# Performance work log

Hardware: AMD Instinct MI355X
Metric: run time of the kernel (lower is better)

The kernel has to match this reference:

```python
import jax, jax.numpy as jnp
import numpy as np

K = 3  # kernel size for all locally-connected layers

def lc2d(x, w, b, stride):
    """Locally connected 2d: per-output-location unshared weights.
    x: [B, C, H, W]; w: [1, O, C, Ho, Wo, K*K]; b: [1, O, Ho, Wo].
    Matches torch: x.unfold(2,K,s).unfold(3,K,s) -> [B,C,Ho,Wo,K,K] flattened
    to K*K, then (x[:,None]*w).sum([2,-1]) + b.
    """
    # patches: [B, C*K*K, Ho, Wo], feature order (c, kh, kw) == torch unfold order
    p = jax.lax.conv_general_dilated_patches(x, (K, K), (stride, stride), 'VALID')
    B, CKK, Ho, Wo = p.shape
    C = w.shape[2]
    p = p.reshape(B, C, K * K, Ho, Wo)
    out = jnp.einsum('bckhw,ochwk->bohw', p, w[0])
    return out + b

def setup_inputs() -> dict:
    key = jax.random.key(0)
    ks = jax.random.split(key, 11)
    s = 0.1
    return {
        'x':   jax.random.normal(ks[0], (8192, 1, 28, 28), dtype=jnp.float32),
        'w1':  jax.random.normal(ks[1], (1, 16, 1, 13, 13, 9), dtype=jnp.float32) * s,
        'b1':  jax.random.normal(ks[2], (1, 16, 13, 13), dtype=jnp.float32) * s,
        'w2':  jax.random.normal(ks[3], (1, 32, 16, 6, 6, 9), dtype=jnp.float32) * s,
        'b2':  jax.random.normal(ks[4], (1, 32, 6, 6), dtype=jnp.float32) * s,
        'w3':  jax.random.normal(ks[5], (1, 64, 32, 4, 4, 9), dtype=jnp.float32) * s,
        'b3':  jax.random.normal(ks[6], (1, 64, 4, 4), dtype=jnp.float32) * s,
        'fw1': jax.random.normal(ks[7], (512, 1024), dtype=jnp.float32) * 0.03,
        'fb1': jax.random.normal(ks[8], (512,), dtype=jnp.float32) * 0.03,
        'fw2': jax.random.normal(ks[9], (10, 512), dtype=jnp.float32) * 0.03,
        'fb2': jax.random.normal(ks[10], (10,), dtype=jnp.float32) * 0.03,
    }

def reference(x, w1, b1, w2, b2, w3, b3, fw1, fb1, fw2, fb2):
    h = jax.nn.relu(lc2d(x, w1, b1, stride=2))   # [B,16,13,13]
    h = jax.nn.relu(lc2d(h, w2, b2, stride=2))   # [B,32,6,6]
    h = lc2d(h, w3, b3, stride=1)                # [B,64,4,4]
    h = h.reshape(h.shape[0], -1)                # [B,1024]
    h = jax.nn.relu(h @ fw1.T + fb1)             # [B,512]
    return h @ fw2.T + fb2                       # [B,10]
```

## Files before the change

kernel.cpp:

```cpp
#include <hip/hip_runtime.h>

typedef __attribute__((ext_vector_type(8))) short short8v;
typedef __attribute__((ext_vector_type(4))) float f32x4;

static __device__ __forceinline__ unsigned short f2bf(float f) {
  union { float f; unsigned u; } v;
  v.f = f;
  const unsigned u = v.u;
  return (unsigned short)((u + 0x7FFF + ((u >> 16) & 1)) >> 16);
}
static __device__ __forceinline__ float bf2f(unsigned short s) {
  union { unsigned u; float f; } v;
  v.u = ((unsigned)s) << 16;
  return v.f;
}


__global__ __launch_bounds__(256) void k_trb(const float* __restrict__ x,
                                             unsigned short* __restrict__ xT,
                                             int Bc) {
  __shared__ float t[32][33];
  const int b0 = blockIdx.x * 32;
  const int f0 = blockIdx.y * 32;
  const int tx = threadIdx.x, ty = threadIdx.y;
  for (int r = ty; r < 32; r += 8) {
    const int f = f0 + tx;
    t[r][tx] = (f < 784) ? x[(size_t)(b0 + r) * 784 + f] : 0.f;
  }
  __syncthreads();
  for (int r = ty; r < 32; r += 8) {
    const int f = f0 + r;
    if (f < 784) xT[(size_t)f * Bc + b0 + tx] = f2bf(t[tx][r]);
  }
}

template <int O, int C, int NPOS, int Kpad>
__global__ void k_wmc(const float* __restrict__ w,
                      unsigned short* __restrict__ wm) {
  const int pos = blockIdx.x, o = blockIdx.y, k = threadIdx.x;
  float v = 0.f;
  if (k < C * 9) {
    const int c = k / 9, kk = k - c * 9;
    v = w[((size_t)(o * C + c) * NPOS + pos) * 9 + kk];
  }
  wm[((size_t)pos * O + o) * Kpad + k] = f2bf(v);
}

__global__ __launch_bounds__(256) void k_wbf(const float* __restrict__ w,
                                             unsigned short* __restrict__ o) {
  const int i = (blockIdx.x * 256 + threadIdx.x) * 8;
  const float4 a = *(const float4*)&w[i];
  const float4 b = *(const float4*)&w[i + 4];
  short8v r;
  r[0] = (short)f2bf(a.x); r[1] = (short)f2bf(a.y);
  r[2] = (short)f2bf(a.z); r[3] = (short)f2bf(a.w);
  r[4] = (short)f2bf(b.x); r[5] = (short)f2bf(b.y);
  r[6] = (short)f2bf(b.z); r[7] = (short)f2bf(b.w);
  *(short8v*)&o[i] = r;
}

template <int O, int K, int NPOS, int HWIN, int WIN, int WOD, int STR,
          bool RELU>
__global__ __launch_bounds__(256) void k_lcm(
    const unsigned short* __restrict__ X, const unsigned short* __restrict__ Wm,
    const float* __restrict__ bias, unsigned short* __restrict__ out, int B) {
  constexpr int NSTEP = (K + 31) / 32;
  constexpr int Kpad = NSTEP * 32;
  constexpr int NBT = (O == 64) ? 8 : ((O == 32) ? 4 : 2);
  __shared__ short Wl[2][O * 40];
  __shared__ short Xl[2][5232];
  __shared__ int rowtab[Kpad];
  const int tid = threadIdx.x;
  const int b0 = blockIdx.x * 128;
  const int pos = blockIdx.y;
  const int ho = pos / WOD, wo = pos - ho * WOD;
  const int w = tid >> 6, l = tid & 63, m = l & 15, g = l >> 4;
  const int jw = (O == 64) ? w * 16 : ((O == 32) ? (w & 1) * 16 : 0);
  const int boff = (O == 64) ? 0 : ((O == 32) ? (w >> 1) * 64 : w * 32);

  for (int k = tid; k < Kpad; k += 256) {
    int r = 0;
    if (k < K) {
      const int c = k / 9, kk = k - c * 9;
      const int kh = kk / 3, kw = kk - kh * 3;
      r = c * HWIN + (ho * STR + kh) * WIN + (wo * STR + kw);
    }
    rowtab[k] = r;
  }
  __syncthreads();

  const unsigned short* wsrc = Wm + (size_t)pos * O * Kpad;
  const int wjj = tid >> 2, wko = (tid & 3) * 8;
  const bool wact = tid < O * 4;
  const int kp = tid >> 4, boct = (tid & 15) * 8;

  f32x4 acc[NBT];
#pragma unroll
  for (int bt = 0; bt < NBT; ++bt) acc[bt] = (f32x4){0.f, 0.f, 0.f, 0.f};

  short8v wreg, xa, xb;
  bool z0, z1;

  if (wact) wreg = *(const short8v*)&wsrc[(size_t)wjj * Kpad + wko];
  {
    const int k0 = 2 * kp;
    z0 = k0 >= K;
    z1 = k0 + 1 >= K;
    if (!z0) xa = *(const short8v*)(X + (size_t)rowtab[k0] * B + b0 + boct);
    if (!z1)
      xb = *(const short8v*)(X + (size_t)rowtab[k0 + 1] * B + b0 + boct);
  }
  if (wact) *(short8v*)&Wl[0][wjj * 40 + wko] = wreg;
  {
    unsigned* xl = (unsigned*)&Xl[0][0];
#pragma unroll
    for (int i = 0; i < 8; ++i) {
      const int b = boct + i;
      const unsigned lo = z0 ? 0u : (unsigned)(unsigned short)xa[i];
      const unsigned hi = z1 ? 0u : (unsigned)(unsigned short)xb[i];
      xl[b * 20 + (b >> 3) * 4 + kp] = lo | (hi << 16);
    }
  }
  __syncthreads();

  for (int t = 0; t < NSTEP; ++t) {
    const int cur = t & 1;
    if (t < NSTEP - 1) {
      const int kc = (t + 1) * 32;
      if (wact) wreg = *(const short8v*)&wsrc[(size_t)wjj * Kpad + kc + wko];
      const int k0 = kc + 2 * kp;
      z0 = k0 >= K;
      z1 = k0 + 1 >= K;
      if (!z0) xa = *(const short8v*)(X + (size_t)rowtab[k0] * B + b0 + boct);
      if (!z1)
        xb = *(const short8v*)(X + (size_t)rowtab[k0 + 1] * B + b0 + boct);
    }
    {
      const short8v aw = *(const short8v*)&Wl[cur][(jw + m) * 40 + g * 8];
      short8v bx[NBT];
#pragma unroll
      for (int bt = 0; bt < NBT; ++bt) {
        const int b = boff + bt * 16 + m;
        bx[bt] = *(const short8v*)&Xl[cur][b * 40 + (b >> 3) * 8 + g * 8];
      }
#pragma unroll
      for (int bt = 0; bt < NBT; ++bt)
        acc[bt] = __builtin_amdgcn_mfma_f32_16x16x32_bf16(aw, bx[bt], acc[bt],
                                                          0, 0, 0);
    }
    if (t < NSTEP - 1) {
      const int nxt = cur ^ 1;
      if (wact) *(short8v*)&Wl[nxt][wjj * 40 + wko] = wreg;
      unsigned* xl = (unsigned*)&Xl[nxt][0];
#pragma unroll
      for (int i = 0; i < 8; ++i) {
        const int b = boct + i;
        const unsigned lo = z0 ? 0u : (unsigned)(unsigned short)xa[i];
        const unsigned hi = z1 ? 0u : (unsigned)(unsigned short)xb[i];
        xl[b * 20 + (b >> 3) * 4 + kp] = lo | (hi << 16);
      }
    }
    __syncthreads();
  }

#pragma unroll
  for (int r = 0; r < 4; ++r) {
    const int o = jw + g * 4 + r;
    const int f = o * NPOS + pos;
    const float bz = bias[f];
#pragma unroll
    for (int bt = 0; bt < NBT; ++bt) {
      float v = acc[bt][r] + bz;
      if (RELU) v = fmaxf(v, 0.f);
      out[(size_t)f * B + b0 + boff + bt * 16 + m] = f2bf(v);
    }
  }
}

__global__ __launch_bounds__(256) void k_fc1m(
    const unsigned short* __restrict__ X,
    const unsigned short* __restrict__ Wbf, const float* __restrict__ fb1,
    unsigned short* __restrict__ out, int B) {
  __shared__ short Wl[2][5120];
  __shared__ short Xl[2][5232];
  const int tid = threadIdx.x;
  const int b0 = blockIdx.x * 128, j0 = blockIdx.y * 128;
  const int w = tid >> 6, l = tid & 63, m = l & 15, g = l >> 4;

  const int wj = tid >> 1, wkh = (tid & 1) * 16;
  const unsigned short* wsrc = Wbf + (size_t)(j0 + wj) * 1024 + wkh;
  const int kp = tid >> 4, boct = (tid & 15) * 8;
  const unsigned short* xsrc = X + (size_t)(2 * kp) * B + b0 + boct;

  f32x4 acc[2][8];
#pragma unroll
  for (int jt = 0; jt < 2; ++jt)
#pragma unroll
    for (int bt = 0; bt < 8; ++bt) acc[jt][bt] = (f32x4){0.f, 0.f, 0.f, 0.f};

  short8v wreg0, wreg1, xa, xb;

  wreg0 = *(const short8v*)(wsrc);
  wreg1 = *(const short8v*)(wsrc + 8);
  xa = *(const short8v*)(xsrc);
  xb = *(const short8v*)(xsrc + B);

  {
    *(short8v*)&Wl[0][wj * 40 + wkh] = wreg0;
    *(short8v*)&Wl[0][wj * 40 + wkh + 8] = wreg1;
    unsigned* xl = (unsigned*)&Xl[0][0];
#pragma unroll
    for (int i = 0; i < 8; ++i) {
      const int b = boct + i;
      xl[b * 20 + (b >> 3) * 4 + kp] = (unsigned)(unsigned short)xa[i] |
                                       ((unsigned)(unsigned short)xb[i] << 16);
    }
  }
  __syncthreads();

  for (int t = 0; t < 32; ++t) {
    const int cur = t & 1;
    if (t < 31) {
      const unsigned short* wp = wsrc + (t + 1) * 32;
      wreg0 = *(const short8v*)(wp);
      wreg1 = *(const short8v*)(wp + 8);
      const unsigned short* xp = xsrc + (size_t)(t + 1) * 32 * B;
      xa = *(const short8v*)(xp);
      xb = *(const short8v*)(xp + B);
    }
    {
      short8v aw[2], bx[8];
#pragma unroll
      for (int jt = 0; jt < 2; ++jt)
        aw[jt] = *(const short8v*)&Wl[cur][(w * 32 + jt * 16 + m) * 40 + g * 8];
#pragma unroll
      for (int bt = 0; bt < 8; ++bt) {
        const int b = bt * 16 + m;
        bx[bt] = *(const short8v*)&Xl[cur][b * 40 + (b >> 3) * 8 + g * 8];
      }
#pragma unroll
      for (int jt = 0; jt < 2; ++jt)
#pragma unroll
        for (int bt = 0; bt < 8; ++bt)
          acc[jt][bt] = __builtin_amdgcn_mfma_f32_16x16x32_bf16(
              aw[jt], bx[bt], acc[jt][bt], 0, 0, 0);
    }
    if (t < 31) {
      const int nxt = cur ^ 1;
      *(short8v*)&Wl[nxt][wj * 40 + wkh] = wreg0;
      *(short8v*)&Wl[nxt][wj * 40 + wkh + 8] = wreg1;
      unsigned* xl = (unsigned*)&Xl[nxt][0];
#pragma unroll
      for (int i = 0; i < 8; ++i) {
        const int b = boct + i;
        xl[b * 20 + (b >> 3) * 4 + kp] =
            (unsigned)(unsigned short)xa[i] |
            ((unsigned)(unsigned short)xb[i] << 16);
      }
    }
    __syncthreads();
  }

#pragma unroll
  for (int jt = 0; jt < 2; ++jt)
#pragma unroll
    for (int r = 0; r < 4; ++r) {
      const int j = j0 + w * 32 + jt * 16 + g * 4 + r;
      const float bj = fb1[j];
#pragma unroll
      for (int bt = 0; bt < 8; ++bt)
        out[(size_t)j * B + b0 + bt * 16 + m] =
            f2bf(fmaxf(acc[jt][bt][r] + bj, 0.f));
    }
}

__global__ __launch_bounds__(256) void k_fc2(
    const unsigned short* __restrict__ in, const float* __restrict__ fw2,
    const float* __restrict__ fb2, float* __restrict__ out, int B, int b0) {
  __shared__ float red[4][10][64];
  const int tx = threadIdx.x;
  const int b = blockIdx.x * 64 + tx;
  const int tyu = threadIdx.y;
  float acc[10];
#pragma unroll
  for (int i = 0; i < 10; ++i) acc[i] = 0.f;
  for (int kk = 0; kk < 128; ++kk) {
    const int k = tyu * 128 + kk;
    const float v = bf2f(in[(size_t)k * B + b]);
#pragma unroll
    for (int i = 0; i < 10; ++i) acc[i] = fmaf(v, fw2[i * 512 + k], acc[i]);
  }
#pragma unroll
  for (int i = 0; i < 10; ++i) red[tyu][i][tx] = acc[i];
  __syncthreads();
  if (threadIdx.y == 0) {
#pragma unroll
    for (int i = 0; i < 10; ++i) {
      const float s = fb2[i] + red[0][i][tx] + red[1][i][tx] + red[2][i][tx] +
                      red[3][i][tx];
      out[(size_t)(b0 + b) * 10 + i] = s;
    }
  }
}

extern "C" void kernel_launch(void* const* d_in, const int* in_sizes, int n_in,
                              void* d_out, int out_size, void* d_ws,
                              size_t ws_size, hipStream_t stream) {
  const float* x   = (const float*)d_in[0];
  const float* w1  = (const float*)d_in[1];
  const float* b1  = (const float*)d_in[2];
  const float* w2  = (const float*)d_in[3];
  const float* b2  = (const float*)d_in[4];
  const float* w3  = (const float*)d_in[5];
  const float* b3  = (const float*)d_in[6];
  const float* fw1 = (const float*)d_in[7];
  const float* fb1 = (const float*)d_in[8];
  const float* fw2 = (const float*)d_in[9];
  const float* fb2 = (const float*)d_in[10];
  float* out = (float*)d_out;

  const int B = in_sizes[0] / 784;

  const size_t nWm1 = (size_t)169 * 16 * 32 / 2;
  const size_t nWm2 = (size_t)36 * 32 * 160 / 2;
  const size_t nWm3 = (size_t)16 * 64 * 288 / 2;
  const size_t nWbf = (size_t)512 * 1024 / 2;
  unsigned short* Wm1 = (unsigned short*)d_ws;
  unsigned short* Wm2 = (unsigned short*)((float*)d_ws + nWm1);
  unsigned short* Wm3 = (unsigned short*)((float*)d_ws + nWm1 + nWm2);
  unsigned short* Wbf = (unsigned short*)((float*)d_ws + nWm1 + nWm2 + nWm3);
  unsigned short* hbase =
      (unsigned short*)((float*)d_ws + nWm1 + nWm2 + nWm3 + nWbf);
  const size_t ws_rem =
      ws_size - (nWm1 + nWm2 + nWm3 + nWbf) * sizeof(float);

  const size_t per_elem = (size_t)(784 + 2704 + 1152 + 1024 + 512) * 2;
  int Bc = B;
  while ((size_t)Bc * per_elem > ws_rem && Bc > 512) Bc >>= 1;
  const int nch = B / Bc;

  unsigned short* XT = hbase;
  unsigned short* H1 = XT + (size_t)784 * Bc;
  unsigned short* H2 = H1 + (size_t)2704 * Bc;
  unsigned short* H3 = H2 + (size_t)1152 * Bc;
  unsigned short* H4 = H3 + (size_t)1024 * Bc;

  k_wmc<16, 1, 169, 32><<<dim3(169, 16), 32, 0, stream>>>(w1, Wm1);
  k_wmc<32, 16, 36, 160><<<dim3(36, 32), 160, 0, stream>>>(w2, Wm2);
  k_wmc<64, 32, 16, 288><<<dim3(16, 64), 288, 0, stream>>>(w3, Wm3);
  k_wbf<<<dim3(256), 256, 0, stream>>>(fw1, Wbf);

  for (int ch = 0; ch < nch; ++ch) {
    const float* xc = x + (size_t)ch * Bc * 784;
    const int b0 = ch * Bc;

    k_trb<<<dim3(Bc / 32, 25), dim3(32, 8), 0, stream>>>(xc, XT, Bc);
    k_lcm<16, 9, 169, 784, 28, 13, 2, true>
        <<<dim3(Bc / 128, 169), 256, 0, stream>>>(XT, Wm1, b1, H1, Bc);
    k_lcm<32, 144, 36, 169, 13, 6, 2, true>
        <<<dim3(Bc / 128, 36), 256, 0, stream>>>(H1, Wm2, b2, H2, Bc);
    k_lcm<64, 288, 16, 36, 6, 4, 1, false>
        <<<dim3(Bc / 128, 16), 256, 0, stream>>>(H2, Wm3, b3, H3, Bc);
    k_fc1m<<<dim3(Bc / 128, 4), 256, 0, stream>>>(H3, Wbf, fb1, H4, Bc);
    k_fc2<<<dim3(Bc / 64), dim3(64, 4), 0, stream>>>(H4, fw2, fb2, out, Bc,
                                                     b0);
  }
}
```

Baseline: 124.9 us.

## Process layer-1 one output row per block using dense banded weights

Replaces the per-position layer-1 locally connected kernel, which had K=9 padded to 32 and covered one output position per block, with a kernel that handles a whole output row (13 positions x 16 channels = 208 outputs) per block. It builds a banded weight matrix over the 3 input rows (84 features padded to 96), so one loaded input slice is reused across all 13 positions. This removes the heavy K padding waste and repeated input loads, at the cost of many zero entries in the banded weights, high accumulator register use (26 f32x4), and larger shared memory. The O==16 branches in the generic kernel are dropped.

```diff
diff --git a/kernel.cpp b/kernel.cpp
--- a/kernel.cpp
+++ b/kernel.cpp
@@ -32,6 +32,20 @@
     const int f = f0 + r;
     if (f < 784) xT[(size_t)f * Bc + b0 + tx] = f2bf(t[tx][r]);
   }
+}
+
+__global__ void k_wd1(const float* __restrict__ w1,
+                      unsigned short* __restrict__ wd) {
+  const int ho = blockIdx.x, f = blockIdx.y, e = threadIdx.x;
+  const int wo = f >> 4, o = f & 15;
+  float v = 0.f;
+  if (e < 84) {
+    const int kh = e / 28, c = e - kh * 28;
+    const int kw = c - 2 * wo;
+    if (kw >= 0 && kw < 3)
+      v = w1[((size_t)o * 169 + ho * 13 + wo) * 9 + kh * 3 + kw];
+  }
+  wd[((size_t)ho * 208 + f) * 96 + e] = f2bf(v);
 }
 
 template <int O, int C, int NPOS, int Kpad>
@@ -59,6 +73,116 @@
   *(short8v*)&o[i] = r;
 }
 
+__global__ __launch_bounds__(256) void k_lc1d(
+    const unsigned short* __restrict__ XT, const unsigned short* __restrict__ Wd,
+    const float* __restrict__ bias, unsigned short* __restrict__ out, int B) {
+  __shared__ short Wl[2][208 * 40];
+  __shared__ short Xl[2][5232];
+  const int tid = threadIdx.x;
+  const int b0 = blockIdx.x * 128;
+  const int ho = blockIdx.y;
+  const int w = tid >> 6, l = tid & 63, m = l & 15, g = l >> 4;
+  const int fbase = 2 * ho * 28;
+
+  const int kp = tid >> 4, boct = (tid & 15) * 8;
+  const unsigned short* xsrc = XT + (size_t)(fbase + 2 * kp) * B + b0 + boct;
+  const unsigned short* wsrc = Wd + (size_t)ho * 208 * 96;
+
+  f32x4 acc[13][2];
+#pragma unroll
+  for (int mt = 0; mt < 13; ++mt)
+#pragma unroll
+    for (int bt = 0; bt < 2; ++bt) acc[mt][bt] = (f32x4){0.f, 0.f, 0.f, 0.f};
+
+  short8v wreg[4], xa, xb;
+#pragma unroll
+  for (int i = 0; i < 4; ++i) {
+    const int c = tid + i * 256;
+    if (c < 832)
+      wreg[i] = *(const short8v*)&wsrc[(size_t)(c >> 2) * 96 + (c & 3) * 8];
+  }
+  xa = *(const short8v*)(xsrc);
+  xb = *(const short8v*)(xsrc + B);
+#pragma unroll
+  for (int i = 0; i < 4; ++i) {
+    const int c = tid + i * 256;
+    if (c < 832) *(short8v*)&Wl[0][(c >> 2) * 40 + (c & 3) * 8] = wreg[i];
+  }
+  {
+    unsigned* xl = (unsigned*)&Xl[0][0];
+#pragma unroll
+    for (int i = 0; i < 8; ++i) {
+      const int b = boct + i;
+      xl[b * 20 + (b >> 3) * 4 + kp] = (unsigned)(unsigned short)xa[i] |
+                                       ((unsigned)(unsigned short)xb[i] << 16);
+    }
+  }
+  __syncthreads();
+
+  for (int t = 0; t < 3; ++t) {
+    const int cur = t & 1;
+    if (t < 2) {
+      const int kc = (t + 1) * 32;
+#pragma unroll
+      for (int i = 0; i < 4; ++i) {
+        const int c = tid + i * 256;
+        if (c < 832)
+          wreg[i] =
+              *(const short8v*)&wsrc[(size_t)(c >> 2) * 96 + kc + (c & 3) * 8];
+      }
+      const unsigned short* xp = xsrc + (size_t)kc * B;
+      xa = *(const short8v*)(xp);
+      xb = *(const short8v*)(xp + B);
+    }
+    {
+      short8v bx[2];
+#pragma unroll
+      for (int bt = 0; bt < 2; ++bt) {
+        const int b = w * 32 + bt * 16 + m;
+        bx[bt] = *(const short8v*)&Xl[cur][b * 40 + (b >> 3) * 8 + g * 8];
+      }
+#pragma unroll
+      for (int mt = 0; mt < 13; ++mt) {
+        const short8v aw = *(const short8v*)&Wl[cur][(mt * 16 + m) * 40 + g * 8];
+        acc[mt][0] =
+            __builtin_amdgcn_mfma_f32_16x16x32_bf16(aw, bx[0], acc[mt][0], 0, 0, 0);
+        acc[mt][1] =
+            __builtin_amdgcn_mfma_f32_16x16x32_bf16(aw, bx[1], acc[mt][1], 0, 0, 0);
+      }
+    }
+    if (t < 2) {
+      const int nxt = cur ^ 1;
+#pragma unroll
+      for (int i = 0; i < 4; ++i) {
+        const int c = tid + i * 256;
+        if (c < 832) *(short8v*)&Wl[nxt][(c >> 2) * 40 + (c & 3) * 8] = wreg[i];
+      }
+      unsigned* xl = (unsigned*)&Xl[nxt][0];
+#pragma unroll
+      for (int i = 0; i < 8; ++i) {
+        const int b = boct + i;
+        xl[b * 20 + (b >> 3) * 4 + kp] =
+            (unsigned)(unsigned short)xa[i] |
+            ((unsigned)(unsigned short)xb[i] << 16);
+      }
+    }
+    __syncthreads();
+  }
+
+#pragma unroll
+  for (int mt = 0; mt < 13; ++mt)
+#pragma unroll
+    for (int r = 0; r < 4; ++r) {
+      const int o = g * 4 + r;
+      const int f = o * 169 + ho * 13 + mt;
+      const float bz = bias[f];
+#pragma unroll
+      for (int bt = 0; bt < 2; ++bt)
+        out[(size_t)f * B + b0 + w * 32 + bt * 16 + m] =
+            f2bf(fmaxf(acc[mt][bt][r] + bz, 0.f));
+    }
+}
+
 template <int O, int K, int NPOS, int HWIN, int WIN, int WOD, int STR,
           bool RELU>
 __global__ __launch_bounds__(256) void k_lcm(
@@ -66,7 +190,7 @@
     const float* __restrict__ bias, unsigned short* __restrict__ out, int B) {
   constexpr int NSTEP = (K + 31) / 32;
   constexpr int Kpad = NSTEP * 32;
-  constexpr int NBT = (O == 64) ? 8 : ((O == 32) ? 4 : 2);
+  constexpr int NBT = (O == 64) ? 8 : 4;
   __shared__ short Wl[2][O * 40];
   __shared__ short Xl[2][5232];
   __shared__ int rowtab[Kpad];
@@ -75,8 +199,8 @@
   const int pos = blockIdx.y;
   const int ho = pos / WOD, wo = pos - ho * WOD;
   const int w = tid >> 6, l = tid & 63, m = l & 15, g = l >> 4;
-  const int jw = (O == 64) ? w * 16 : ((O == 32) ? (w & 1) * 16 : 0);
-  const int boff = (O == 64) ? 0 : ((O == 32) ? (w >> 1) * 64 : w * 32);
+  const int jw = (O == 64) ? w * 16 : (w & 1) * 16;
+  const int boff = (O == 64) ? 0 : (w >> 1) * 64;
 
   for (int k = tid; k < Kpad; k += 256) {
     int r = 0;
@@ -321,18 +445,18 @@
 
   const int B = in_sizes[0] / 784;
 
-  const size_t nWm1 = (size_t)169 * 16 * 32 / 2;
+  const size_t nWd1 = (size_t)13 * 208 * 96 / 2;
   const size_t nWm2 = (size_t)36 * 32 * 160 / 2;
   const size_t nWm3 = (size_t)16 * 64 * 288 / 2;
   const size_t nWbf = (size_t)512 * 1024 / 2;
-  unsigned short* Wm1 = (unsigned short*)d_ws;
-  unsigned short* Wm2 = (unsigned short*)((float*)d_ws + nWm1);
-  unsigned short* Wm3 = (unsigned short*)((float*)d_ws + nWm1 + nWm2);
-  unsigned short* Wbf = (unsigned short*)((float*)d_ws + nWm1 + nWm2 + nWm3);
+  unsigned short* Wd1 = (unsigned short*)d_ws;
+  unsigned short* Wm2 = (unsigned short*)((float*)d_ws + nWd1);
+  unsigned short* Wm3 = (unsigned short*)((float*)d_ws + nWd1 + nWm2);
+  unsigned short* Wbf = (unsigned short*)((float*)d_ws + nWd1 + nWm2 + nWm3);
   unsigned short* hbase =
-      (unsigned short*)((float*)d_ws + nWm1 + nWm2 + nWm3 + nWbf);
+      (unsigned short*)((float*)d_ws + nWd1 + nWm2 + nWm3 + nWbf);
   const size_t ws_rem =
-      ws_size - (nWm1 + nWm2 + nWm3 + nWbf) * sizeof(float);
+      ws_size - (nWd1 + nWm2 + nWm3 + nWbf) * sizeof(float);
 
   const size_t per_elem = (size_t)(784 + 2704 + 1152 + 1024 + 512) * 2;
   int Bc = B;
@@ -345,7 +469,7 @@
   unsigned short* H3 = H2 + (size_t)1152 * Bc;
   unsigned short* H4 = H3 + (size_t)1024 * Bc;
 
-  k_wmc<16, 1, 169, 32><<<dim3(169, 16), 32, 0, stream>>>(w1, Wm1);
+  k_wd1<<<dim3(13, 208), 96, 0, stream>>>(w1, Wd1);
   k_wmc<32, 16, 36, 160><<<dim3(36, 32), 160, 0, stream>>>(w2, Wm2);
   k_wmc<64, 32, 16, 288><<<dim3(16, 64), 288, 0, stream>>>(w3, Wm3);
   k_wbf<<<dim3(256), 256, 0, stream>>>(fw1, Wbf);
@@ -355,8 +479,7 @@
     const int b0 = ch * Bc;
 
     k_trb<<<dim3(Bc / 32, 25), dim3(32, 8), 0, stream>>>(xc, XT, Bc);
-    k_lcm<16, 9, 169, 784, 28, 13, 2, true>
-        <<<dim3(Bc / 128, 169), 256, 0, stream>>>(XT, Wm1, b1, H1, Bc);
+    k_lc1d<<<dim3(Bc / 128, 13), 256, 0, stream>>>(XT, Wd1, b1, H1, Bc);
     k_lcm<32, 144, 36, 169, 13, 6, 2, true>
         <<<dim3(Bc / 128, 36), 256, 0, stream>>>(H1, Wm2, b2, H2, Bc);
     k_lcm<64, 288, 16, 36, 6, 4, 1, false>
```

New measurement: 128.0 us. 1.03x slower.
